# Kernel tuning notes

Measured on AMD Instinct MI355X. Metric: run time of the kernel, lower is better.

Reference implementation:

```python
import jax, jax.numpy as jnp
import numpy as np

N_NODES = 50000
N_EDGES = 800000


def _gcn_conv(x, W, b, src, dst, norm, n_nodes):
    # PyG GCNConv: out = D^{-1/2} (A + I) D^{-1/2} (x W) + b
    h = x @ W                                  # [N, out]
    msg = h[src] * norm[:, None]               # [E+N, out] gathered, normalized messages
    agg = jax.ops.segment_sum(msg, dst, num_segments=n_nodes)
    return agg + b


def _build_norm(edge_index, n_nodes):
    # add self-loops, compute symmetric degree normalization
    loop = jnp.arange(n_nodes, dtype=edge_index.dtype)
    src = jnp.concatenate([edge_index[0], loop])
    dst = jnp.concatenate([edge_index[1], loop])
    deg = jnp.zeros((n_nodes,), jnp.float32).at[dst].add(1.0)
    dinv = jnp.where(deg > 0, jax.lax.rsqrt(deg), 0.0)
    norm = dinv[src] * dinv[dst]
    return src, dst, norm


def setup_inputs() -> dict:
    key = jax.random.key(0)
    ks = jax.random.split(key, 5)
    x = jax.random.normal(ks[0], (N_NODES, 128), dtype=jnp.float32)
    edge_index = jax.random.randint(ks[1], (2, N_EDGES), 0, N_NODES, dtype=jnp.int64)
    s1 = 1.0 / np.sqrt(128)
    s2 = 1.0 / np.sqrt(128)
    s3 = 1.0 / np.sqrt(64)
    return {
        "x": x,
        "edge_index": edge_index,
        "W1": jax.random.normal(ks[2], (128, 128), dtype=jnp.float32) * s1,
        "b1": jnp.zeros((128,), jnp.float32),
        "W2": jax.random.normal(ks[3], (128, 64), dtype=jnp.float32) * s2,
        "b2": jnp.zeros((64,), jnp.float32),
        "W3": jax.random.normal(ks[4], (64, 128), dtype=jnp.float32) * s3,
        "b3": jnp.zeros((128,), jnp.float32),
    }


def reference(x, edge_index, W1, b1, W2, b2, W3, b3):
    n = x.shape[0]
    src, dst, norm = _build_norm(edge_index, n)
    # dropout is identity in eval mode
    h = jax.nn.relu(_gcn_conv(x, W1, b1, src, dst, norm, n))
    h = jax.nn.relu(_gcn_conv(h, W2, b2, src, dst, norm, n))
    out = _gcn_conv(h, W3, b3, src, dst, norm, n)
    return out
```

## Files before the change

kernel.cpp:

```cpp
#include <hip/hip_runtime.h>


#define DEV_INLINE __device__ __forceinline__

typedef unsigned int uint;
typedef unsigned short ushort;
typedef __attribute__((ext_vector_type(8))) short bf16x8;
typedef __attribute__((ext_vector_type(4))) float f32x4;

static DEV_INLINE uint f2bf_rne(float f) {
    uint u = __float_as_uint(f);
    return (u + 0x7FFFu + ((u >> 16) & 1u)) >> 16;
}
static DEV_INLINE float bflo(uint u) { return __uint_as_float(u << 16); }
static DEV_INLINE float bfhi(uint u) { return __uint_as_float(u & 0xFFFF0000u); }

static DEV_INLINE void fma8(float4& a, float4& b, float n, const uint4& v) {
    a.x = fmaf(n, bflo(v.x), a.x); a.y = fmaf(n, bfhi(v.x), a.y);
    a.z = fmaf(n, bflo(v.y), a.z); a.w = fmaf(n, bfhi(v.y), a.w);
    b.x = fmaf(n, bflo(v.z), b.x); b.y = fmaf(n, bfhi(v.z), b.y);
    b.z = fmaf(n, bflo(v.w), b.z); b.w = fmaf(n, bfhi(v.w), b.w);
}

static DEV_INLINE void split8(const float4& x0, const float4& x1, bf16x8& ah, bf16x8& al) {
    float xs[8] = {x0.x, x0.y, x0.z, x0.w, x1.x, x1.y, x1.z, x1.w};
#pragma unroll
    for (int j = 0; j < 8; ++j) {
        uint u = __float_as_uint(xs[j]);
        ah[j] = (short)(u >> 16);
        float r = xs[j] - __uint_as_float(u & 0xFFFF0000u);
        al[j] = (short)(__float_as_uint(r) >> 16);
    }
}


template<int K, int NOUT>
static DEV_INLINE void prep_one(const float* __restrict__ W,
                                ushort* __restrict__ Wh, ushort* __restrict__ Wl, int id) {
    constexpr int C = NOUT / 16;
    int lane = id & 63;
    int tc   = id >> 6;
    int c = tc % C, t = tc / C;
    int krow = t * 32 + (lane >> 4) * 8;
    int col  = c * 16 + (lane & 15);
#pragma unroll
    for (int j = 0; j < 8; ++j) {
        float w = W[(size_t)(krow + j) * NOUT + col];
        uint u = __float_as_uint(w);
        Wh[(size_t)id * 8 + j] = (ushort)(u >> 16);
        float r = w - __uint_as_float(u & 0xFFFF0000u);
        Wl[(size_t)id * 8 + j] = (ushort)(__float_as_uint(r) >> 16);
    }
}

__global__ __launch_bounds__(256) void prep_zero_kernel(
    const float* __restrict__ W1, const float* __restrict__ W2, const float* __restrict__ W3,
    ushort* w1h, ushort* w1l, ushort* w2h, ushort* w2l, ushort* w3h, ushort* w3l,
    int* __restrict__ cnt, int NBK2)
{
    const int bid = blockIdx.x, tid = threadIdx.x;
    if (bid < 16) {
        int id = bid * 256 + tid;
        if (id < 2048)       prep_one<128, 128>(W1, w1h, w1l, id);
        else if (id < 3072)  prep_one<128, 64>(W2, w2h, w2l, id - 2048);
        else if (id < 4096)  prep_one<64, 128>(W3, w3h, w3l, id - 3072);
    } else {
        for (int j = tid; j < NBK2; j += 256) cnt[j] = 0;
    }
}


__global__ __launch_bounds__(256) void hist_kernel(
    const int* __restrict__ dst, int* __restrict__ cnt, int E, int NBK2)
{
    __shared__ int h[512];
    const int tid = threadIdx.x, bid = blockIdx.x, G = gridDim.x;
    for (int j = tid; j < NBK2; j += 256) h[j] = 0;
    __syncthreads();
    for (int i = bid * 256 + tid; i < E; i += G * 256)
        atomicAdd(&h[dst[i] >> 7], 1);
    __syncthreads();
    for (int j = tid; j < NBK2; j += 256) {
        int v = h[j];
        if (v) atomicAdd(&cnt[j], v);
    }
}

__global__ __launch_bounds__(256) void scan_kernel(
    const int* __restrict__ cnt, int* __restrict__ base, int* __restrict__ cursor,
    int* __restrict__ rowptr, int NBK2, int N, int E)
{
    __shared__ int buf[512];
    const int tid = threadIdx.x;
    for (int j = tid; j < 512; j += 256) buf[j] = (j < NBK2) ? cnt[j] : 0;
    __syncthreads();
    for (int ofs = 1; ofs < 256; ofs <<= 1) {
        int a = (tid >= ofs) ? buf[tid - ofs] : 0;
        int b = (tid >= ofs) ? buf[256 + tid - ofs] : 0;
        __syncthreads();
        buf[tid] += a; buf[256 + tid] += b;
        __syncthreads();
    }
    int tot0 = buf[255];
    for (int j = tid; j < NBK2; j += 256) {
        int incl = buf[j] + ((j >= 256) ? tot0 : 0);
        int ex = incl - cnt[j];
        base[j] = ex; cursor[j] = ex;
    }
    if (tid == 0) rowptr[N] = E;
}


template<int K, int NOUT, bool ABF, bool POSTB, bool OUTBF>
static DEV_INLINE void gemm_body(const void* __restrict__ A,
                                 const ushort* __restrict__ Whf, const ushort* __restrict__ Wlf,
                                 const float* __restrict__ bias_n,
                                 void* __restrict__ Cout, int N, int vt, int tid)
{
    constexpr int C  = NOUT / 16;
    constexpr int T  = K / 32;
    const int w    = tid >> 6;
    const int lane = tid & 63;
    const int row0 = vt * 64 + w * 16;

    const int arow  = row0 + (lane & 15);
    const int arowc = (arow < N) ? arow : (N - 1);
    const int lq    = (lane >> 4);

    const bf16x8* WH = reinterpret_cast<const bf16x8*>(Whf);
    const bf16x8* WL = reinterpret_cast<const bf16x8*>(Wlf);

    f32x4 acc[C];
#pragma unroll
    for (int c = 0; c < C; ++c) acc[c] = (f32x4){0.f, 0.f, 0.f, 0.f};

#pragma unroll
    for (int t = 0; t < T; ++t) {
        bf16x8 ah, al;
        if (ABF) {
            const ushort* ap = (const ushort*)A + (size_t)arowc * K + t * 32 + lq * 8;
            ah = *reinterpret_cast<const bf16x8*>(ap);
        } else {
            const float* ap = (const float*)A + (size_t)arowc * K + t * 32 + lq * 8;
            float4 x0 = *reinterpret_cast<const float4*>(ap);
            float4 x1 = *reinterpret_cast<const float4*>(ap + 4);
            split8(x0, x1, ah, al);
        }
#pragma unroll
        for (int c = 0; c < C; ++c) {
            bf16x8 bh = WH[(t * C + c) * 64 + lane];
            bf16x8 bl = WL[(t * C + c) * 64 + lane];
            acc[c] = __builtin_amdgcn_mfma_f32_16x16x32_bf16(ah, bh, acc[c], 0, 0, 0);
            if (!ABF)
                acc[c] = __builtin_amdgcn_mfma_f32_16x16x32_bf16(al, bh, acc[c], 0, 0, 0);
            acc[c] = __builtin_amdgcn_mfma_f32_16x16x32_bf16(ah, bl, acc[c], 0, 0, 0);
        }
    }

    const int rbase = (lane >> 4) * 4;
    const int ccol  = (lane & 15);
#pragma unroll
    for (int r = 0; r < 4; ++r) {
        int row = row0 + rbase + r;
        if (row < N) {
#pragma unroll
            for (int c = 0; c < C; ++c) {
                int col = c * 16 + ccol;
                float v = acc[c][r];
                if (POSTB) v += bias_n[col];
                if (OUTBF) ((ushort*)Cout)[(size_t)row * NOUT + col] = (ushort)f2bf_rne(v);
                else       ((float*)Cout)[(size_t)row * NOUT + col] = v;
            }
        }
    }
}

__global__ __launch_bounds__(256) void scatter_gemm1_kernel(
    const int* __restrict__ src, const int* __restrict__ dst,
    int* __restrict__ cursor, uint* __restrict__ pkg, int E, int NBK2, int nchunks,
    const float* __restrict__ x, const ushort* __restrict__ w1h,
    const ushort* __restrict__ w1l, ushort* __restrict__ H1, int N)
{
    __shared__ int S[1024];
    const int bid = blockIdx.x, tid = threadIdx.x;
    if (bid < nchunks) {
        int* histL = S;
        int* baseL = S + 512;
        const int c0 = bid * 2048;
        for (int j = tid; j < NBK2; j += 256) histL[j] = 0;
        __syncthreads();
#pragma unroll
        for (int k = 0; k < 8; ++k) {
            int idx = c0 + k * 256 + tid;
            if (idx < E) atomicAdd(&histL[dst[idx] >> 7], 1);
        }
        __syncthreads();
        for (int j = tid; j < NBK2; j += 256) {
            int h = histL[j];
            baseL[j] = h ? atomicAdd(&cursor[j], h) : 0;
            histL[j] = 0;
        }
        __syncthreads();
#pragma unroll
        for (int k = 0; k < 8; ++k) {
            int idx = c0 + k * 256 + tid;
            if (idx < E) {
                int d = dst[idx];
                int b = d >> 7;
                int pos = baseL[b] + atomicAdd(&histL[b], 1);
                pkg[pos] = ((uint)d << 16) | (uint)(src[idx] & 0xFFFF);
            }
        }
    } else {
        gemm_body<128, 128, false, false, true>(x, w1h, w1l, nullptr, H1, N,
                                                bid - nchunks, tid);
    }
}

__global__ __launch_bounds__(256) void build_kernel(
    const uint* __restrict__ pkg, const int* __restrict__ cnt,
    const int* __restrict__ base392, int* __restrict__ rowptr,
    float* __restrict__ dinv, ushort* __restrict__ perm, int N)
{
    __shared__ uint S[6400];
    uint*   pkL  = S;
    ushort* outS = (ushort*)(S + 4096);
    int*    hist = (int*)(S + 6144);
    int*    buf  = (int*)(S + 6272);
    const int vb = blockIdx.x, tid = threadIdx.x;
    const int base = base392[vb];
    int nE = cnt[vb]; if (nE > 4096) nE = 4096;

    if (tid < 128) hist[tid] = 0;
    __syncthreads();
    for (int i = tid; i < nE; i += 256) {
        uint pk = pkg[base + i];
        pkL[i] = pk;
        atomicAdd(&hist[(pk >> 16) & 127], 1);
    }
    __syncthreads();
    if (tid < 128) buf[tid] = hist[tid];
    __syncthreads();
    for (int ofs = 1; ofs < 128; ofs <<= 1) {
        int t = (tid < 128 && tid >= ofs) ? buf[tid - ofs] : 0;
        __syncthreads();
        if (tid < 128) buf[tid] += t;
        __syncthreads();
    }
    if (tid < 128) {
        int c = hist[tid];
        int ex = buf[tid] - c;
        int node = vb * 128 + tid;
        if (node < N) {
            rowptr[node] = base + ex;
            dinv[node]   = rsqrtf((float)(c + 1));
        }
        hist[tid] = ex;
    }
    __syncthreads();
    for (int i = tid; i < nE; i += 256) {
        uint pk = pkL[i];
        int pos = atomicAdd(&hist[(pk >> 16) & 127], 1);
        outS[pos] = (ushort)(pk & 0xFFFFu);
    }
    __syncthreads();
    for (int i = tid; i < nE; i += 256) perm[base + i] = outS[i];
}


template<int K, int NOUT, bool ABF, bool POSTB, bool OUTBF>
__global__ __launch_bounds__(256) void gemm_kernel(
    const void* __restrict__ A, const ushort* __restrict__ Wh, const ushort* __restrict__ Wl,
    const float* __restrict__ bn, void* __restrict__ C, int N)
{
    gemm_body<K, NOUT, ABF, POSTB, OUTBF>(A, Wh, Wl, bn, C, N, blockIdx.x, threadIdx.x);
}


template<int F, bool BIAS, bool RELU, bool OUTBF>
__global__ __launch_bounds__(256) void agg_gather_kernel(
    const uint* __restrict__ H, const int* __restrict__ rowptr,
    const ushort* __restrict__ perm_src, const float* __restrict__ dinv,
    const float* __restrict__ bias, void* __restrict__ OUT, int N)
{
    constexpr int GROUP = F / 8;
    constexpr int FW    = F / 2;
    constexpr int NPB   = 256 / GROUP;
    const int lane = threadIdx.x % GROUP;
    const int g    = threadIdx.x / GROUP;
    const int node = blockIdx.x * NPB + g;
    if (node >= N) return;

    const int beg = rowptr[node];
    const int end = rowptr[node + 1];
    const float di = dinv[node];

    float4 aA = make_float4(0.f, 0.f, 0.f, 0.f), aB = aA;
    float4 bA = aA, bB = aA;
    {
        uint4 v = reinterpret_cast<const uint4*>(H + (size_t)node * FW)[lane];
        fma8(aA, aB, di * di, v);
    }

    int e = beg;
    for (; e + 3 < end; e += 4) {
        int s0 = perm_src[e];     int s1 = perm_src[e + 1];
        int s2 = perm_src[e + 2]; int s3 = perm_src[e + 3];
        float n0 = dinv[s0] * di, n1 = dinv[s1] * di;
        float n2 = dinv[s2] * di, n3 = dinv[s3] * di;
        uint4 v0 = reinterpret_cast<const uint4*>(H + (size_t)s0 * FW)[lane];
        uint4 v1 = reinterpret_cast<const uint4*>(H + (size_t)s1 * FW)[lane];
        uint4 v2 = reinterpret_cast<const uint4*>(H + (size_t)s2 * FW)[lane];
        uint4 v3 = reinterpret_cast<const uint4*>(H + (size_t)s3 * FW)[lane];
        fma8(aA, aB, n0, v0);
        fma8(bA, bB, n1, v1);
        fma8(aA, aB, n2, v2);
        fma8(bA, bB, n3, v3);
    }
    for (; e < end; ++e) {
        int s0 = perm_src[e];
        float n0 = dinv[s0] * di;
        uint4 v0 = reinterpret_cast<const uint4*>(H + (size_t)s0 * FW)[lane];
        fma8(aA, aB, n0, v0);
    }
    aA.x += bA.x; aA.y += bA.y; aA.z += bA.z; aA.w += bA.w;
    aB.x += bB.x; aB.y += bB.y; aB.z += bB.z; aB.w += bB.w;

    if (BIAS) {
        const float4* b4 = reinterpret_cast<const float4*>(bias);
        float4 c0 = b4[lane * 2], c1 = b4[lane * 2 + 1];
        aA.x += c0.x; aA.y += c0.y; aA.z += c0.z; aA.w += c0.w;
        aB.x += c1.x; aB.y += c1.y; aB.z += c1.z; aB.w += c1.w;
    }
    if (RELU) {
        aA.x = fmaxf(aA.x, 0.f); aA.y = fmaxf(aA.y, 0.f);
        aA.z = fmaxf(aA.z, 0.f); aA.w = fmaxf(aA.w, 0.f);
        aB.x = fmaxf(aB.x, 0.f); aB.y = fmaxf(aB.y, 0.f);
        aB.z = fmaxf(aB.z, 0.f); aB.w = fmaxf(aB.w, 0.f);
    }

    if (OUTBF) {
        uint4 u;
        u.x = f2bf_rne(aA.x) | (f2bf_rne(aA.y) << 16);
        u.y = f2bf_rne(aA.z) | (f2bf_rne(aA.w) << 16);
        u.z = f2bf_rne(aB.x) | (f2bf_rne(aB.y) << 16);
        u.w = f2bf_rne(aB.z) | (f2bf_rne(aB.w) << 16);
        reinterpret_cast<uint4*>((uint*)OUT + (size_t)node * FW)[lane] = u;
    } else {
        float4* O = reinterpret_cast<float4*>((float*)OUT + (size_t)node * F);
        O[lane * 2]     = aA;
        O[lane * 2 + 1] = aB;
    }
}


static inline size_t align_up(size_t v, size_t a) { return (v + a - 1) / a * a; }

extern "C" void kernel_launch(void* const* d_in, const int* in_sizes, int n_in,
                              void* d_out, int out_size, void* d_ws, size_t ws_size,
                              hipStream_t stream) {
    const float* x  = (const float*)d_in[0];
    const int*   ei = (const int*)d_in[1];
    const float* W1 = (const float*)d_in[2];
    const float* b1 = (const float*)d_in[3];
    const float* W2 = (const float*)d_in[4];
    const float* b2 = (const float*)d_in[5];
    const float* W3 = (const float*)d_in[6];
    const float* b3 = (const float*)d_in[7];
    float* out = (float*)d_out;

    const int N = in_sizes[0] / 128;
    const int E = in_sizes[1] / 2;
    const int* src = ei;
    const int* dst = ei + E;
    const int NBK2    = (N + 127) / 128;
    const int nchunks = (E + 2047) / 2048;
    const int gRow    = (N + 63) / 64;

    char* ws = (char*)d_ws;
    size_t off = 0;
    float* dinv    = (float*)(ws + off); off = align_up(off + (size_t)N * 4, 512);
    int*   rowptr  = (int*)  (ws + off); off = align_up(off + (size_t)(N + 1) * 4, 512);
    int*   cnt     = (int*)  (ws + off); off = align_up(off + (size_t)NBK2 * 4, 512);
    int*   base392 = (int*)  (ws + off); off = align_up(off + (size_t)NBK2 * 4, 512);
    int*   cursor  = (int*)  (ws + off); off = align_up(off + (size_t)NBK2 * 4, 512);
    ushort* perm   = (ushort*)(ws + off); off = align_up(off + (size_t)E * 2, 512);
    uint*  pkg     = (uint*) (ws + off); off = align_up(off + (size_t)E * 4, 512);
    uint*  regA    = (uint*) (ws + off); off = align_up(off + (size_t)N * 64 * 4, 512);
    uint*  regB    = (uint*) (ws + off); off = align_up(off + (size_t)N * 64 * 4, 512);
    ushort* w1h = (ushort*)(ws + off); off = align_up(off + (size_t)128 * 128 * 2, 512);
    ushort* w1l = (ushort*)(ws + off); off = align_up(off + (size_t)128 * 128 * 2, 512);
    ushort* w2h = (ushort*)(ws + off); off = align_up(off + (size_t)128 * 64 * 2, 512);
    ushort* w2l = (ushort*)(ws + off); off = align_up(off + (size_t)128 * 64 * 2, 512);
    ushort* w3h = (ushort*)(ws + off); off = align_up(off + (size_t)64 * 128 * 2, 512);
    ushort* w3l = (ushort*)(ws + off); off = align_up(off + (size_t)64 * 128 * 2, 512);
    (void)ws_size;

    uint*  H1bf = regA;
    uint*  AGG1 = regB;
    uint*  H2bf = regA;
    uint*  H3bf = regA + (size_t)N * 32;
    float* T    = (float*)regB;

    dim3 blk(256);

    prep_zero_kernel<<<17, blk, 0, stream>>>(W1, W2, W3, w1h, w1l, w2h, w2l, w3h, w3l,
                                             cnt, NBK2);
    hist_kernel<<<392, blk, 0, stream>>>(dst, cnt, E, NBK2);
    scan_kernel<<<1, blk, 0, stream>>>(cnt, base392, cursor, rowptr, NBK2, N, E);
    scatter_gemm1_kernel<<<nchunks + gRow, blk, 0, stream>>>(
        src, dst, cursor, pkg, E, NBK2, nchunks, x, w1h, w1l, (ushort*)H1bf, N);
    build_kernel<<<NBK2, blk, 0, stream>>>(pkg, cnt, base392, rowptr, dinv, perm, N);
    agg_gather_kernel<128, true, true, true><<<(N + 15) / 16, blk, 0, stream>>>(
        H1bf, rowptr, perm, dinv, b1, AGG1, N);
    gemm_kernel<128, 64, true, false, true><<<gRow, blk, 0, stream>>>(
        AGG1, w2h, w2l, nullptr, H2bf, N);
    agg_gather_kernel<64, true, true, true><<<(N + 31) / 32, blk, 0, stream>>>(
        H2bf, rowptr, perm, dinv, b2, H3bf, N);
    agg_gather_kernel<64, false, false, false><<<(N + 31) / 32, blk, 0, stream>>>(
        H3bf, rowptr, perm, dinv, nullptr, T, N);
    gemm_kernel<64, 128, false, true, false><<<gRow, blk, 0, stream>>>(
        T, w3h, w3l, b3, out, N);
}
```

Baseline: 220.4 us.

## Replace histogram+scan with fixed-capacity per-bucket edge storage

Removes the global histogram and scan kernels by giving each 128-node bucket a fixed slot of BCAP entries, using atomic counters directly as cursors. Rows are described by separate begin/end arrays, since buckets are no longer contiguous. This cuts two launches and a serialized single-block scan. Edges beyond the capacity of a bucket are dropped, so correctness depends on degree distribution, and the workspace grows.

New measurement: 213.1 us. 3.3% less time.

```diff
diff --git a/kernel.cpp b/kernel.cpp
--- a/kernel.cpp
+++ b/kernel.cpp
@@ -7,6 +7,8 @@
 typedef unsigned short ushort;
 typedef __attribute__((ext_vector_type(8))) short bf16x8;
 typedef __attribute__((ext_vector_type(4))) float f32x4;
+
+#define BCAP 4096
 
 static DEV_INLINE uint f2bf_rne(float f) {
     uint u = __float_as_uint(f);
@@ -67,47 +69,6 @@
     } else {
         for (int j = tid; j < NBK2; j += 256) cnt[j] = 0;
     }
-}
-
-
-__global__ __launch_bounds__(256) void hist_kernel(
-    const int* __restrict__ dst, int* __restrict__ cnt, int E, int NBK2)
-{
-    __shared__ int h[512];
-    const int tid = threadIdx.x, bid = blockIdx.x, G = gridDim.x;
-    for (int j = tid; j < NBK2; j += 256) h[j] = 0;
-    __syncthreads();
-    for (int i = bid * 256 + tid; i < E; i += G * 256)
-        atomicAdd(&h[dst[i] >> 7], 1);
-    __syncthreads();
-    for (int j = tid; j < NBK2; j += 256) {
-        int v = h[j];
-        if (v) atomicAdd(&cnt[j], v);
-    }
-}
-
-__global__ __launch_bounds__(256) void scan_kernel(
-    const int* __restrict__ cnt, int* __restrict__ base, int* __restrict__ cursor,
-    int* __restrict__ rowptr, int NBK2, int N, int E)
-{
-    __shared__ int buf[512];
-    const int tid = threadIdx.x;
-    for (int j = tid; j < 512; j += 256) buf[j] = (j < NBK2) ? cnt[j] : 0;
-    __syncthreads();
-    for (int ofs = 1; ofs < 256; ofs <<= 1) {
-        int a = (tid >= ofs) ? buf[tid - ofs] : 0;
-        int b = (tid >= ofs) ? buf[256 + tid - ofs] : 0;
-        __syncthreads();
-        buf[tid] += a; buf[256 + tid] += b;
-        __syncthreads();
-    }
-    int tot0 = buf[255];
-    for (int j = tid; j < NBK2; j += 256) {
-        int incl = buf[j] + ((j >= 256) ? tot0 : 0);
-        int ex = incl - cnt[j];
-        base[j] = ex; cursor[j] = ex;
-    }
-    if (tid == 0) rowptr[N] = E;
 }
 
 
@@ -177,7 +138,7 @@
 
 __global__ __launch_bounds__(256) void scatter_gemm1_kernel(
     const int* __restrict__ src, const int* __restrict__ dst,
-    int* __restrict__ cursor, uint* __restrict__ pkg, int E, int NBK2, int nchunks,
+    int* __restrict__ cnt, uint* __restrict__ pkg, int E, int NBK2, int nchunks,
     const float* __restrict__ x, const ushort* __restrict__ w1h,
     const ushort* __restrict__ w1l, ushort* __restrict__ H1, int N)
 {
@@ -197,7 +158,7 @@
         __syncthreads();
         for (int j = tid; j < NBK2; j += 256) {
             int h = histL[j];
-            baseL[j] = h ? atomicAdd(&cursor[j], h) : 0;
+            baseL[j] = h ? atomicAdd(&cnt[j], h) : 0;
             histL[j] = 0;
         }
         __syncthreads();
@@ -208,7 +169,8 @@
                 int d = dst[idx];
                 int b = d >> 7;
                 int pos = baseL[b] + atomicAdd(&histL[b], 1);
-                pkg[pos] = ((uint)d << 16) | (uint)(src[idx] & 0xFFFF);
+                if (pos < BCAP)
+                    pkg[(size_t)b * BCAP + pos] = ((uint)d << 16) | (uint)(src[idx] & 0xFFFF);
             }
         }
     } else {
@@ -219,7 +181,7 @@
 
 __global__ __launch_bounds__(256) void build_kernel(
     const uint* __restrict__ pkg, const int* __restrict__ cnt,
-    const int* __restrict__ base392, int* __restrict__ rowptr,
+    int* __restrict__ rowbeg, int* __restrict__ rowend,
     float* __restrict__ dinv, ushort* __restrict__ perm, int N)
 {
     __shared__ uint S[6400];
@@ -228,8 +190,8 @@
     int*    hist = (int*)(S + 6144);
     int*    buf  = (int*)(S + 6272);
     const int vb = blockIdx.x, tid = threadIdx.x;
-    const int base = base392[vb];
-    int nE = cnt[vb]; if (nE > 4096) nE = 4096;
+    const int base = vb * BCAP;
+    int nE = cnt[vb]; if (nE > BCAP) nE = BCAP;
 
     if (tid < 128) hist[tid] = 0;
     __syncthreads();
@@ -252,7 +214,8 @@
         int ex = buf[tid] - c;
         int node = vb * 128 + tid;
         if (node < N) {
-            rowptr[node] = base + ex;
+            rowbeg[node] = base + ex;
+            rowend[node] = base + ex + c;
             dinv[node]   = rsqrtf((float)(c + 1));
         }
         hist[tid] = ex;
@@ -279,9 +242,10 @@
 
 template<int F, bool BIAS, bool RELU, bool OUTBF>
 __global__ __launch_bounds__(256) void agg_gather_kernel(
-    const uint* __restrict__ H, const int* __restrict__ rowptr,
-    const ushort* __restrict__ perm_src, const float* __restrict__ dinv,
-    const float* __restrict__ bias, void* __restrict__ OUT, int N)
+    const uint* __restrict__ H, const int* __restrict__ rowbeg,
+    const int* __restrict__ rowend, const ushort* __restrict__ perm_src,
+    const float* __restrict__ dinv, const float* __restrict__ bias,
+    void* __restrict__ OUT, int N)
 {
     constexpr int GROUP = F / 8;
     constexpr int FW    = F / 2;
@@ -291,8 +255,8 @@
     const int node = blockIdx.x * NPB + g;
     if (node >= N) return;
 
-    const int beg = rowptr[node];
-    const int end = rowptr[node + 1];
+    const int beg = rowbeg[node];
+    const int end = rowend[node];
     const float di = dinv[node];
 
     float4 aA = make_float4(0.f, 0.f, 0.f, 0.f), aB = aA;
@@ -380,12 +344,11 @@
     char* ws = (char*)d_ws;
     size_t off = 0;
     float* dinv    = (float*)(ws + off); off = align_up(off + (size_t)N * 4, 512);
-    int*   rowptr  = (int*)  (ws + off); off = align_up(off + (size_t)(N + 1) * 4, 512);
+    int*   rowbeg  = (int*)  (ws + off); off = align_up(off + (size_t)N * 4, 512);
+    int*   rowend  = (int*)  (ws + off); off = align_up(off + (size_t)N * 4, 512);
     int*   cnt     = (int*)  (ws + off); off = align_up(off + (size_t)NBK2 * 4, 512);
-    int*   base392 = (int*)  (ws + off); off = align_up(off + (size_t)NBK2 * 4, 512);
-    int*   cursor  = (int*)  (ws + off); off = align_up(off + (size_t)NBK2 * 4, 512);
-    ushort* perm   = (ushort*)(ws + off); off = align_up(off + (size_t)E * 2, 512);
-    uint*  pkg     = (uint*) (ws + off); off = align_up(off + (size_t)E * 4, 512);
+    ushort* perm   = (ushort*)(ws + off); off = align_up(off + (size_t)NBK2 * BCAP * 2, 512);
+    uint*  pkg     = (uint*) (ws + off); off = align_up(off + (size_t)NBK2 * BCAP * 4, 512);
     uint*  regA    = (uint*) (ws + off); off = align_up(off + (size_t)N * 64 * 4, 512);
     uint*  regB    = (uint*) (ws + off); off = align_up(off + (size_t)N * 64 * 4, 512);
     ushort* w1h = (ushort*)(ws + off); off = align_up(off + (size_t)128 * 128 * 2, 512);
@@ -406,19 +369,17 @@
 
     prep_zero_kernel<<<17, blk, 0, stream>>>(W1, W2, W3, w1h, w1l, w2h, w2l, w3h, w3l,
                                              cnt, NBK2);
-    hist_kernel<<<392, blk, 0, stream>>>(dst, cnt, E, NBK2);
-    scan_kernel<<<1, blk, 0, stream>>>(cnt, base392, cursor, rowptr, NBK2, N, E);
     scatter_gemm1_kernel<<<nchunks + gRow, blk, 0, stream>>>(
-        src, dst, cursor, pkg, E, NBK2, nchunks, x, w1h, w1l, (ushort*)H1bf, N);
-    build_kernel<<<NBK2, blk, 0, stream>>>(pkg, cnt, base392, rowptr, dinv, perm, N);
+        src, dst, cnt, pkg, E, NBK2, nchunks, x, w1h, w1l, (ushort*)H1bf, N);
+    build_kernel<<<NBK2, blk, 0, stream>>>(pkg, cnt, rowbeg, rowend, dinv, perm, N);
     agg_gather_kernel<128, true, true, true><<<(N + 15) / 16, blk, 0, stream>>>(
-        H1bf, rowptr, perm, dinv, b1, AGG1, N);
+        H1bf, rowbeg, rowend, perm, dinv, b1, AGG1, N);
     gemm_kernel<128, 64, true, false, true><<<gRow, blk, 0, stream>>>(
         AGG1, w2h, w2l, nullptr, H2bf, N);
     agg_gather_kernel<64, true, true, true><<<(N + 31) / 32, blk, 0, stream>>>(
-        H2bf, rowptr, perm, dinv, b2, H3bf, N);
+        H2bf, rowbeg, rowend, perm, dinv, b2, H3bf, N);
     agg_gather_kernel<64, false, false, false><<<(N + 31) / 32, blk, 0, stream>>>(
-        H3bf, rowptr, perm, dinv, nullptr, T, N);
+        H3bf, rowbeg, rowend, perm, dinv, nullptr, T, N);
     gemm_kernel<64, 128, false, true, false><<<gRow, blk, 0, stream>>>(
         T, w3h, w3l, b3, out, N);
 }
```
